# Optimization experiments

Hardware: AMD Instinct MI355X
Metric: run time of the kernel (lower is better)

Reference implementation:

```python
import jax, jax.numpy as jnp
import numpy as np

N_QUBITS = 12
N_LAYERS = 4
BATCH = 4096
DIM = 2 ** N_QUBITS  # 4096


def _apply_1q(state, U, q):
    """Apply 2x2 complex gate U to qubit q. state: (B,) + (2,)*n, wire 0 = MSB (axis q+1)."""
    state = jnp.moveaxis(state, q + 1, -1)
    state = state @ U.T
    return jnp.moveaxis(state, -1, q + 1)


def _apply_cnot(state, c, t):
    """CNOT with control c, target t: flip target amplitudes where control bit == 1."""
    flipped = jnp.flip(state, axis=t + 1)
    shape = [2 if i == c + 1 else 1 for i in range(state.ndim)]
    ctrl = jnp.arange(2).reshape(shape)
    return jnp.where(ctrl == 1, flipped, state)


def setup_inputs() -> dict:
    key = jax.random.key(0)
    k1, k2 = jax.random.split(key)
    x = jax.random.normal(k1, (BATCH, DIM), dtype=jnp.float32)
    weights = jax.random.normal(k2, (N_LAYERS, N_QUBITS, 2), dtype=jnp.float32) * 0.1
    return {"x": x, "weights": weights}


def reference(x, weights):
    n, L = N_QUBITS, N_LAYERS
    B = x.shape[0]
    # AmplitudeEmbedding with normalize=True
    norm = jnp.linalg.norm(x, axis=-1, keepdims=True)
    state = (x / norm).astype(jnp.complex64).reshape((B,) + (2,) * n)
    for layer in range(L):
        for q in range(n):
            ty = weights[layer, q, 0]
            tz = weights[layer, q, 1]
            c, s = jnp.cos(ty / 2), jnp.sin(ty / 2)
            em = jnp.exp(-0.5j * tz.astype(jnp.complex64))  # e^{-i tz/2}
            ep = jnp.exp(+0.5j * tz.astype(jnp.complex64))
            # U = RZ(tz) @ RY(ty), fused single 2x2 gate per qubit
            U = jnp.stack([
                jnp.stack([c * em, -s * em]),
                jnp.stack([s * ep, c * ep]),
            ]).astype(jnp.complex64)
            state = _apply_1q(state, U, q)
        for q in range(n - 1):
            state = _apply_cnot(state, q, q + 1)
        if n > 2:
            state = _apply_cnot(state, n - 1, 0)
    probs = jnp.abs(state) ** 2  # (B,) + (2,)*n, float32
    reduce_axes = tuple(range(1, probs.ndim))
    outs = []
    for q in range(n):
        shape = [2 if i == q + 1 else 1 for i in range(probs.ndim)]
        sign = jnp.array([1.0, -1.0], dtype=probs.dtype).reshape(shape)
        outs.append(jnp.sum(probs * sign, axis=reduce_axes))
    return jnp.stack(outs, axis=-1)  # (B, n_qubits) <Z_q> expvals
```

## Files before the change

kernel.cpp:

```cpp
#include <hip/hip_runtime.h>

#define NQ   12
#define DIM  4096
#define NL   4
#define BLK  256

typedef unsigned short u16;
typedef unsigned int   u32;
typedef float f2 __attribute__((ext_vector_type(2)));
typedef float f4v __attribute__((ext_vector_type(4)));

struct L12 { u16 b[NQ]; };

static constexpr u32 lap(const L12& A, u32 x){ u32 r=0; for(int p=0;p<NQ;++p) if((x>>p)&1u) r^=A.b[p]; return r; }
static constexpr L12 lcomp(const L12& A, const L12& B){ L12 r{}; for(int p=0;p<NQ;++p) r.b[p]=(u16)lap(A,(u32)B.b[p]); return r; }
static constexpr L12 lident(){ L12 r{}; for(int p=0;p<NQ;++p) r.b[p]=(u16)(1u<<p); return r; }

static constexpr u32 applyT(u32 i){
  i ^= ((i>>0)&1u) << 11;
  for(int q=10;q>=0;--q){ int pc=11-q, pt=10-q; i ^= ((i>>pc)&1u) << pt; }
  return i;
}
static constexpr L12 lT(){ L12 t{}; for(int p=0;p<NQ;++p) t.b[p]=(u16)applyT(1u<<p); return t; }

static constexpr L12 linv(const L12& A){
  u16 v[NQ]; u16 u[NQ];
  for(int p=0;p<NQ;++p){ v[p]=A.b[p]; u[p]=(u16)(1u<<p); }
  for(int t=0;t<NQ;++t){
    int p=t; while(!((v[p]>>t)&1u)) ++p;
    u16 tv=v[p]; v[p]=v[t]; v[t]=tv; u16 tu=u[p]; u[p]=u[t]; u[t]=tu;
    for(int k=0;k<NQ;++k) if(k!=t && ((v[k]>>t)&1u)){ v[k]^=v[t]; u[k]^=u[t]; }
  }
  L12 r{}; for(int p=0;p<NQ;++p) r.b[p]=u[p]; return r;
}
static constexpr L12 ltr(const L12& A){
  L12 r{}; for(int p=0;p<NQ;++p) for(int q=0;q<NQ;++q) if((A.b[p]>>q)&1u) r.b[q]=(u16)(r.b[q]|(1u<<p));
  return r;
}
static constexpr int cpop(u32 v){ int n=0; while(v){ n+=(int)(v&1u); v>>=1; } return n; }

struct Tables {
  u16 cm[12][16];
  u16 wg[12][4];
  u16 sp[12][4];
  u16 wexp[NQ];
};

static constexpr Tables make_tables(){
  Tables tb{};
  const L12 T   = lT();
  const L12 Tit = ltr(linv(T));
  L12 A = lident();
  L12 W = lident();
  for(int l=0;l<NL;++l){
    for(int g=0;g<3;++g){
      const int st = l*3+g;
      u16 mm[4]={0,0,0,0};
      for(int i=0;i<4;++i){ mm[i]=A.b[4*g+i]; tb.wg[st][i]=W.b[4*g+i]; }
      u32 ech[4]={0,0,0,0}; int piv[4]={0,0,0,0};
      for(int i=0;i<4;++i){
        u32 v=mm[i];
        for(int k=0;k<i;++k) if((v>>piv[k])&1u) v^=ech[k];
        int t2=11; while(!((v>>t2)&1u)) --t2;
        piv[i]=t2; ech[i]=v;
      }
      for(int a2=0;a2<4;++a2) for(int b2=a2+1;b2<4;++b2)
        if(piv[b2]<piv[a2]){ int tt=piv[a2]; piv[a2]=piv[b2]; piv[b2]=tt; }
      for(int i=0;i<4;++i) tb.sp[st][i]=(u16)piv[i];
      for(int c=0;c<16;++c){ u32 m=0; for(int i=0;i<4;++i) if((c>>i)&1) m^=mm[i]; tb.cm[st][c]=(u16)m; }
    }
    A = lcomp(A, T);
    W = lcomp(W, Tit);
  }
  for(int p=0;p<NQ;++p) tb.wexp[p]=W.b[p];
  return tb;
}

static constexpr u16 UIMG[12] = {1,2,4,8, 3,5,6,7, 9,10,11,13};

static constexpr u32 swz(u32 j){
  u32 f=0;
  for(int k=4;k<12;++k) if((j>>k)&1u) f ^= (u32)UIMG[k];
  return j ^ (f & 15u);
}

static constexpr int rankbits(const u16* v, int n, u16 mask){
  u16 bas[4]={0,0,0,0}; int r=0;
  for(int i=0;i<n;++i){
    u16 x=(u16)(v[i]&mask);
    for(int it=0; it<5 && x; ++it){
      int hb=3; while(hb>0 && !((x>>hb)&1u)) --hb;
      if(bas[hb]) x=(u16)(x^bas[hb]); else { bas[hb]=x; ++r; x=0; }
    }
  }
  return r;
}

struct Derived {
  u32 lane_c[12][8];
  u32 smb[12][4];
  u32 scmb[12][16];
  u32 g0lane[8];
  u32 u11lane[8];
  u32 u11smb[4];
  u16 pm[12];
  u16 mu[12];
};

static constexpr Derived make_derived(){
  const Tables tb = make_tables();
  Derived d{};
  for(int st=0; st<12; ++st){
    bool isp[12]={false,false,false,false,false,false,false,false,false,false,false,false};
    for(int i=0;i<4;++i) isp[tb.sp[st][i]]=true;
    int np[8]; int nn=0;
    for(int p=0;p<12;++p) if(!isp[p]) np[nn++]=p;
    u16 img8[8];
    for(int j=0;j<8;++j) img8[j]=(u16)(swz(1u<<np[j])&15u);
    int ord[8]={0,1,2,3,4,5,6,7}; bool okf=false;
    for(int a=0;a<8&&!okf;++a)for(int b=a+1;b<8&&!okf;++b)
    for(int c2=b+1;c2<8&&!okf;++c2)for(int dd=c2+1;dd<8&&!okf;++dd){
      u16 four[4]={img8[a],img8[b],img8[c2],img8[dd]};
      if(rankbits(four,4,15)!=4) continue;
      const int ids[4]={a,b,c2,dd};
      for(int ex=0; ex<4 && !okf; ++ex){
        u16 tri[3]; int tj=0;
        for(int j=0;j<4;++j) if(j!=ex) tri[tj++]=four[j];
        if(rankbits(tri,3,7)!=3) continue;
        int pp=0;
        for(int j=0;j<4;++j) if(j!=ex) ord[pp++]=ids[j];
        ord[3]=ids[ex];
        int rp=4;
        for(int j=0;j<8;++j){
          bool used=false; for(int k2=0;k2<4;++k2) if(ids[k2]==j) used=true;
          if(!used) ord[rp++]=j;
        }
        okf=true;
      }
    }
    for(int k=0;k<8;++k){
      const int pos = np[ord[k]];
      const u32 addr = swz(1u<<pos)<<4;
      u32 nib=0;
      for(int i=0;i<4;++i) nib |= (u32)((tb.wg[st][i]>>pos)&1u)<<i;
      d.lane_c[st][k] = addr | (nib<<28);
      if(st==0)  d.g0lane[k]  = 1u<<pos;
      if(st==11) d.u11lane[k] = 1u<<pos;
    }
    for(int i=0;i<4;++i)  d.smb[st][i]  = swz((u32)tb.cm[st][1<<i])<<4;
    for(int c=0;c<16;++c) d.scmb[st][c] = swz((u32)tb.cm[st][c])<<4;
    if(st==11) for(int i=0;i<4;++i) d.u11smb[i] = (u32)tb.cm[11][1<<i];
  }
  for(int q=0;q<12;++q){
    d.pm[q] = tb.wexp[11-q];
    u32 m=0;
    for(int i=0;i<4;++i) m |= (u32)(cpop((u32)tb.cm[11][1u<<i] & (u32)tb.wexp[11-q])&1)<<i;
    d.mu[q]=(u16)m;
  }
  return d;
}

__device__ constexpr Derived DV = make_derived();

__device__ __forceinline__ f2 pkfma(f2 a, f2 b, f2 c){
  f2 d;
  asm("v_pk_fma_f32 %0, %1, %2, %3" : "=v"(d) : "v"(a), "v"(b), "v"(c));
  return d;
}

template<int ST, bool WITHW>
__device__ __forceinline__ void gates(f2 (&R)[16], f2 (&I)[16], const float4* __restrict__ gw){
#pragma unroll
  for(int i=0;i<4;++i){
    const float4 g = gw[ST*4+i];
    const f2 mt  = {g.x, g.x};
    const f2 sy  = {g.y, g.y};
    const f2 mgz = {g.z, g.z};
    const f2 sw  = {g.w, g.w};
#pragma unroll
    for(int c=0;c<16;++c){
      if((c>>i)&1) continue;
      const int c1 = c|(1<<i);
      f2 uR = pkfma(mt, R[c1], R[c]);
      f2 uI = pkfma(mt, I[c1], I[c]);
      f2 vR = pkfma(sy, uR, R[c1]);
      f2 vI = pkfma(sy, uI, I[c1]);
      R[c] = pkfma(mt, vR, uR);
      I[c] = pkfma(mt, vI, uI);
      if(WITHW){
        const f2 tr = pkfma(mgz, vI, vR);
        vI = pkfma(sw, tr, vI);
        vR = pkfma(mgz, vI, tr);
      }
      R[c1]=vR; I[c1]=vI;
    }
  }
}

template<int ST, bool WITHW>
__device__ __forceinline__ void mid_step(const u32* msk, char* lds, const float4* __restrict__ gw){
  u32 acc=0;
#pragma unroll
  for(int k=0;k<8;++k) acc ^= DV.lane_c[ST][k]&msk[k];
  const u32 nib = acc>>28;
  u32 base = acc & 0x0FFFFFFFu;
#pragma unroll
  for(int i=0;i<4;++i) base ^= DV.smb[ST][i] & (0u-((nib>>i)&1u));
  u32 ad[16]; f2 R[16], I[16];
#pragma unroll
  for(int c=0;c<16;++c){
    ad[c] = base ^ DV.scmb[ST][c];
    const f4v v = *(const f4v*)(lds+ad[c]);
    R[c]=v.lo; I[c]=v.hi;
  }
  gates<ST,WITHW>(R,I,gw);
#pragma unroll
  for(int c=0;c<16;++c){ f4v v; v.lo=R[c]; v.hi=I[c]; *(f4v*)(lds+ad[c]) = v; }
  __syncthreads();
}

__global__ void prep_kernel(const float* __restrict__ w, float4* __restrict__ gw){
  const int t = threadIdx.x;
  if(t < NL*NQ){
    const int l=t/NQ, p=t%NQ, q=(NQ-1)-p;
    const float ty=w[(l*NQ+q)*2+0], tz=w[(l*NQ+q)*2+1];
    gw[t]=make_float4(-tanf(0.25f*ty), sinf(0.5f*ty), -tanf(0.5f*tz), sinf(tz));
  }
}

__global__ __launch_bounds__(BLK, 2) void qsim_kernel(const float* __restrict__ x,
                                                      const float4* __restrict__ gw,
                                                      float* __restrict__ out)
{
  __shared__ f4v st4[DIM];
  char* lds = (char*)st4;
  const int tid = threadIdx.x;
  const int bb  = blockIdx.x;

  u32 msk[8];
#pragma unroll
  for(int k=0;k<8;++k) msk[k]=0u-((u32)(tid>>k)&1u);

  u32 rep0=0, acc0=0;
#pragma unroll
  for(int k=0;k<8;++k){ rep0 ^= DV.g0lane[k]&msk[k]; acc0 ^= DV.lane_c[0][k]&msk[k]; }
  const u32 base0 = acc0 & 0x0FFFFFFFu;

  f2 R[16], I[16];
  const float* xr0 = x + (size_t)(2*bb)*DIM + rep0;
  const float* xr1 = xr0 + DIM;
#pragma unroll
  for(int s=0;s<4;++s){
    const float4 v0 = *reinterpret_cast<const float4*>(xr0 + 4*s);
    const float4 v1 = *reinterpret_cast<const float4*>(xr1 + 4*s);
    R[4*s+0]=(f2){v0.x,v1.x}; R[4*s+1]=(f2){v0.y,v1.y};
    R[4*s+2]=(f2){v0.z,v1.z}; R[4*s+3]=(f2){v0.w,v1.w};
    I[4*s+0]=(f2){0.f,0.f};   I[4*s+1]=(f2){0.f,0.f};
    I[4*s+2]=(f2){0.f,0.f};   I[4*s+3]=(f2){0.f,0.f};
  }
  gates<0,true>(R,I,gw);
#pragma unroll
  for(int c=0;c<16;++c){ f4v v; v.lo=R[c]; v.hi=I[c];
    *(f4v*)(lds + (base0 ^ DV.scmb[0][c])) = v; }
  __syncthreads();

  mid_step<1,true >(msk,lds,gw);
  mid_step<2,true >(msk,lds,gw);
  mid_step<3,true >(msk,lds,gw);
  mid_step<4,true >(msk,lds,gw);
  mid_step<5,true >(msk,lds,gw);
  mid_step<6,true >(msk,lds,gw);
  mid_step<7,true >(msk,lds,gw);
  mid_step<8,true >(msk,lds,gw);
  mid_step<9,false>(msk,lds,gw);
  mid_step<10,false>(msk,lds,gw);

  {
    u32 acc=0, urep=0;
#pragma unroll
    for(int k=0;k<8;++k){ acc ^= DV.lane_c[11][k]&msk[k]; urep ^= DV.u11lane[k]&msk[k]; }
    const u32 nib = acc>>28;
    u32 base = acc & 0x0FFFFFFFu;
#pragma unroll
    for(int i=0;i<4;++i){ const u32 mi=0u-((nib>>i)&1u); base ^= DV.smb[11][i]&mi; urep ^= DV.u11smb[i]&mi; }
#pragma unroll
    for(int c=0;c<16;++c){
      const f4v v = *(const f4v*)(lds + (base ^ DV.scmb[11][c]));
      R[c]=v.lo; I[c]=v.hi;
    }
    gates<11,false>(R,I,gw);

    f2 pr[16];
#pragma unroll
    for(int c=0;c<16;++c) pr[c]=pkfma(R[c],R[c], pkfma(I[c],I[c],(f2){0.f,0.f}));
    const f2 mone = {-1.f,-1.f};
#pragma unroll
    for(int b=1;b<16;b<<=1){
#pragma unroll
      for(int c=0;c<16;++c){
        if(c&b) continue;
        const f2 u=pr[c], v=pr[c|b];
        pr[c]=u+v;
        pr[c|b]=pkfma(v,mone,u);
      }
    }
    f2 accq[12];
#pragma unroll
    for(int q=0;q<12;++q){
      const u32 sb = ((u32)__popc(urep & (u32)DV.pm[q]) & 1u)<<31;
      const f2 a = pr[DV.mu[q]];
      accq[q]=(f2){__uint_as_float(__float_as_uint(a.x)^sb),
                   __uint_as_float(__float_as_uint(a.y)^sb)};
    }
    f2 nrm2 = pr[0];
#pragma unroll
    for(int o=32;o;o>>=1){
      nrm2.x += __shfl_xor(nrm2.x,o);
      nrm2.y += __shfl_xor(nrm2.y,o);
#pragma unroll
      for(int q=0;q<12;++q){
        accq[q].x += __shfl_xor(accq[q].x,o);
        accq[q].y += __shfl_xor(accq[q].y,o);
      }
    }
    __syncthreads();
    f2* wredp = (f2*)lds;
    const int wid=tid>>6;
    if((tid&63)==0){
#pragma unroll
      for(int q=0;q<12;++q) wredp[wid*13+q]=accq[q];
      wredp[wid*13+12]=nrm2;
    }
    __syncthreads();
    if(tid<NQ){
      const f2 s0=wredp[0*13+tid]+wredp[1*13+tid]+wredp[2*13+tid]+wredp[3*13+tid];
      const f2 sn=wredp[0*13+12]+wredp[1*13+12]+wredp[2*13+12]+wredp[3*13+12];
      out[(size_t)(2*bb+0)*NQ+tid]=s0.x/sn.x;
      out[(size_t)(2*bb+1)*NQ+tid]=s0.y/sn.y;
    }
  }
}

extern "C" void kernel_launch(void* const* d_in, const int* in_sizes, int n_in,
                              void* d_out, int out_size, void* d_ws, size_t ws_size,
                              hipStream_t stream) {
  const float* x = (const float*)d_in[0];
  const float* w = (const float*)d_in[1];
  float* out = (float*)d_out;
  float4* gw = (float4*)d_ws;
  const int B = in_sizes[0] / DIM;
  prep_kernel<<<1, 64, 0, stream>>>(w, gw);
  qsim_kernel<<<B/2, BLK, 0, stream>>>(x, gw, out);
}
```

Baseline: 114.9 us.

## Split each 4-qubit stage across lane pairs with DPP exchange, 512 threads

Each thread now holds 8 amplitudes instead of 16 and the block grows to 512 threads. One of the four qubits per stage is mapped to adjacent lanes, and its gate is applied with DPP quad-permute exchanges plus a lane-dependent sign. The aim is to cut register pressure and raise occupancy and parallelism. In exchange it adds per-stage cross-lane traffic, extra multiplies for the lane gate, and twice as many waves taking part in each barrier. Packed FMA inline asm is also replaced with elementwise fma builtins.

```diff
diff --git a/kernel.cpp b/kernel.cpp
--- a/kernel.cpp
+++ b/kernel.cpp
@@ -3,7 +3,7 @@
 #define NQ   12
 #define DIM  4096
 #define NL   4
-#define BLK  256
+#define BLK  512
 
 typedef unsigned short u16;
 typedef unsigned int   u32;
@@ -97,12 +97,13 @@
 }
 
 struct Derived {
-  u32 lane_c[12][8];
-  u32 smb[12][4];
-  u32 scmb[12][16];
-  u32 g0lane[8];
-  u32 u11lane[8];
-  u32 u11smb[4];
+  u32 lane_c[12][9];
+  u32 smb[12][3];
+  u32 scmb[12][8];
+  u32 g0lane[9];
+  u32 u0smb[3];
+  u32 u11lane[9];
+  u32 u11smb[3];
   u16 pm[12];
   u16 mu[12];
 };
@@ -110,51 +111,52 @@
 static constexpr Derived make_derived(){
   const Tables tb = make_tables();
   Derived d{};
+  u16 mm11[4]={0,0,0,0};
   for(int st=0; st<12; ++st){
+    u16 mm[4];
+    for(int i=0;i<4;++i) mm[i]=tb.cm[st][1u<<i];
+    if(st==11) for(int i=0;i<4;++i) mm11[i]=mm[i];
     bool isp[12]={false,false,false,false,false,false,false,false,false,false,false,false};
     for(int i=0;i<4;++i) isp[tb.sp[st][i]]=true;
     int np[8]; int nn=0;
     for(int p=0;p<12;++p) if(!isp[p]) np[nn++]=p;
-    u16 img8[8];
-    for(int j=0;j<8;++j) img8[j]=(u16)(swz(1u<<np[j])&15u);
-    int ord[8]={0,1,2,3,4,5,6,7}; bool okf=false;
-    for(int a=0;a<8&&!okf;++a)for(int b=a+1;b<8&&!okf;++b)
-    for(int c2=b+1;c2<8&&!okf;++c2)for(int dd=c2+1;dd<8&&!okf;++dd){
-      u16 four[4]={img8[a],img8[b],img8[c2],img8[dd]};
-      if(rankbits(four,4,15)!=4) continue;
-      const int ids[4]={a,b,c2,dd};
-      for(int ex=0; ex<4 && !okf; ++ex){
-        u16 tri[3]; int tj=0;
-        for(int j=0;j<4;++j) if(j!=ex) tri[tj++]=four[j];
-        if(rankbits(tri,3,7)!=3) continue;
-        int pp=0;
-        for(int j=0;j<4;++j) if(j!=ex) ord[pp++]=ids[j];
-        ord[3]=ids[ex];
-        int rp=4;
-        for(int j=0;j<8;++j){
-          bool used=false; for(int k2=0;k2<4;++k2) if(ids[k2]==j) used=true;
-          if(!used) ord[rp++]=j;
-        }
-        okf=true;
-      }
-    }
-    for(int k=0;k<8;++k){
-      const int pos = np[ord[k]];
-      const u32 addr = swz(1u<<pos)<<4;
+    u16 img[8];
+    for(int j=0;j<8;++j) img[j]=(u16)(swz(1u<<np[j])&15u);
+    const u16 img0=(u16)(swz((u32)mm[3])&15u);
+    int b1=0,b2=1,b3=2,best=-1;
+    for(int i1=0;i1<8;++i1)for(int i2=0;i2<8;++i2)for(int i3=0;i3<8;++i3){
+      if(i1==i2||i1==i3||i2==i3) continue;
+      u16 t8[3]={img0,img[i1],img[i2]};
+      u16 t16[4]={img0,img[i1],img[i2],img[i3]};
+      const int sc = rankbits(t16,4,15)*10 + rankbits(t8,3,7);
+      if(sc>best){ best=sc; b1=i1;b2=i2;b3=i3; }
+    }
+    int ord[8]={b1,b2,b3,0,0,0,0,0}; int rp=3;
+    for(int j=0;j<8;++j){ if(j!=b1&&j!=b2&&j!=b3) ord[rp++]=j; }
+    d.lane_c[st][0] = (swz((u32)mm[3])<<4) | (8u<<28);
+    if(st==0)  d.g0lane[0]=(u32)mm[3];
+    if(st==11) d.u11lane[0]=(u32)mm[3];
+    for(int k=1;k<9;++k){
+      const int pos=np[ord[k-1]];
       u32 nib=0;
-      for(int i=0;i<4;++i) nib |= (u32)((tb.wg[st][i]>>pos)&1u)<<i;
-      d.lane_c[st][k] = addr | (nib<<28);
-      if(st==0)  d.g0lane[k]  = 1u<<pos;
-      if(st==11) d.u11lane[k] = 1u<<pos;
-    }
-    for(int i=0;i<4;++i)  d.smb[st][i]  = swz((u32)tb.cm[st][1<<i])<<4;
-    for(int c=0;c<16;++c) d.scmb[st][c] = swz((u32)tb.cm[st][c])<<4;
-    if(st==11) for(int i=0;i<4;++i) d.u11smb[i] = (u32)tb.cm[11][1<<i];
+      for(int i=0;i<4;++i) nib|=(u32)((tb.wg[st][i]>>pos)&1u)<<i;
+      d.lane_c[st][k]=(swz(1u<<pos)<<4)|(nib<<28);
+      if(st==0)  d.g0lane[k]=1u<<pos;
+      if(st==11) d.u11lane[k]=1u<<pos;
+    }
+    for(int i=0;i<3;++i) d.smb[st][i]=swz((u32)mm[i])<<4;
+    for(int c=0;c<8;++c){
+      u32 m=0;
+      for(int i=0;i<3;++i) if((c>>i)&1) m^=(u32)mm[i];
+      d.scmb[st][c]=swz(m)<<4;
+    }
+    if(st==0)  for(int i=0;i<3;++i) d.u0smb[i]=(u32)mm[i];
+    if(st==11) for(int i=0;i<3;++i) d.u11smb[i]=(u32)mm[i];
   }
   for(int q=0;q<12;++q){
-    d.pm[q] = tb.wexp[11-q];
+    d.pm[q]=tb.wexp[11-q];
     u32 m=0;
-    for(int i=0;i<4;++i) m |= (u32)(cpop((u32)tb.cm[11][1u<<i] & (u32)tb.wexp[11-q])&1)<<i;
+    for(int i=0;i<3;++i) m|=(u32)(cpop((u32)mm11[i]&(u32)tb.wexp[11-q])&1)<<i;
     d.mu[q]=(u16)m;
   }
   return d;
@@ -162,35 +164,31 @@
 
 __device__ constexpr Derived DV = make_derived();
 
-__device__ __forceinline__ f2 pkfma(f2 a, f2 b, f2 c){
-  f2 d;
-  asm("v_pk_fma_f32 %0, %1, %2, %3" : "=v"(d) : "v"(a), "v"(b), "v"(c));
-  return d;
-}
+__device__ __forceinline__ float dppx(float v){
+  return __int_as_float(__builtin_amdgcn_mov_dpp(__float_as_int(v), 0xB1, 0xF, 0xF, true));
+}
+__device__ __forceinline__ f2 dpp2(f2 v){ f2 r; r.x=dppx(v.x); r.y=dppx(v.y); return r; }
 
 template<int ST, bool WITHW>
-__device__ __forceinline__ void gates(f2 (&R)[16], f2 (&I)[16], const float4* __restrict__ gw){
-#pragma unroll
-  for(int i=0;i<4;++i){
-    const float4 g = gw[ST*4+i];
-    const f2 mt  = {g.x, g.x};
-    const f2 sy  = {g.y, g.y};
-    const f2 mgz = {g.z, g.z};
-    const f2 sw  = {g.w, g.w};
-#pragma unroll
-    for(int c=0;c<16;++c){
+__device__ __forceinline__ void reg_gates(f2 (&R)[8], f2 (&I)[8], const float4* __restrict__ gwS){
+#pragma unroll
+  for(int i=0;i<3;++i){
+    const float4 g = gwS[ST*4+i];
+    const f2 mt={g.x,g.x}, sy={g.y,g.y}, mtz={-g.z,-g.z}, sz={g.w,g.w};
+#pragma unroll
+    for(int c=0;c<8;++c){
       if((c>>i)&1) continue;
-      const int c1 = c|(1<<i);
-      f2 uR = pkfma(mt, R[c1], R[c]);
-      f2 uI = pkfma(mt, I[c1], I[c]);
-      f2 vR = pkfma(sy, uR, R[c1]);
-      f2 vI = pkfma(sy, uI, I[c1]);
-      R[c] = pkfma(mt, vR, uR);
-      I[c] = pkfma(mt, vI, uI);
+      const int c1=c|(1<<i);
+      f2 uR=__builtin_elementwise_fma(mt,R[c1],R[c]);
+      f2 uI=__builtin_elementwise_fma(mt,I[c1],I[c]);
+      f2 vR=__builtin_elementwise_fma(sy,uR,R[c1]);
+      f2 vI=__builtin_elementwise_fma(sy,uI,I[c1]);
+      R[c]=__builtin_elementwise_fma(mt,vR,uR);
+      I[c]=__builtin_elementwise_fma(mt,vI,uI);
       if(WITHW){
-        const f2 tr = pkfma(mgz, vI, vR);
-        vI = pkfma(sw, tr, vI);
-        vR = pkfma(mgz, vI, tr);
+        f2 t=__builtin_elementwise_fma(mtz,vI,vR);
+        vI=__builtin_elementwise_fma(sz,t,vI);
+        vR=__builtin_elementwise_fma(mtz,vI,t);
       }
       R[c1]=vR; I[c1]=vI;
     }
@@ -198,38 +196,66 @@
 }
 
 template<int ST, bool WITHW>
-__device__ __forceinline__ void mid_step(const u32* msk, char* lds, const float4* __restrict__ gw){
+__device__ __forceinline__ void lane_gate(f2 (&R)[8], f2 (&I)[8], const float4* __restrict__ gwD, u32 r3m){
+  const float4 g = gwD[ST];
+  const float sg = __uint_as_float(__float_as_uint(g.y) ^ r3m ^ 0x80000000u);
+  const f2 vcy={g.x,g.x}, vsy={sg,sg};
+  const float en = r3m ? 1.f : 0.f;
+  const f2 vmtz={-g.z*en,-g.z*en}, vsz={g.w*en,g.w*en};
+#pragma unroll
+  for(int c=0;c<8;++c){
+    const f2 Rp=dpp2(R[c]), Ip=dpp2(I[c]);
+    f2 nR=__builtin_elementwise_fma(vcy,R[c],vsy*Rp);
+    f2 nI=__builtin_elementwise_fma(vcy,I[c],vsy*Ip);
+    if(WITHW){
+      f2 t=__builtin_elementwise_fma(vmtz,nI,nR);
+      nI=__builtin_elementwise_fma(vsz,t,nI);
+      nR=__builtin_elementwise_fma(vmtz,nI,t);
+    }
+    R[c]=nR; I[c]=nI;
+  }
+}
+
+template<int ST, bool WITHW>
+__device__ __forceinline__ void mid_step(const u32* msk, char* lds,
+                                         const float4* __restrict__ gwS,
+                                         const float4* __restrict__ gwD){
   u32 acc=0;
 #pragma unroll
-  for(int k=0;k<8;++k) acc ^= DV.lane_c[ST][k]&msk[k];
+  for(int k=0;k<9;++k) acc ^= DV.lane_c[ST][k]&msk[k];
   const u32 nib = acc>>28;
   u32 base = acc & 0x0FFFFFFFu;
 #pragma unroll
-  for(int i=0;i<4;++i) base ^= DV.smb[ST][i] & (0u-((nib>>i)&1u));
-  u32 ad[16]; f2 R[16], I[16];
-#pragma unroll
-  for(int c=0;c<16;++c){
-    ad[c] = base ^ DV.scmb[ST][c];
-    const f4v v = *(const f4v*)(lds+ad[c]);
+  for(int i=0;i<3;++i) base ^= DV.smb[ST][i] & (0u-((nib>>i)&1u));
+  const u32 r3m = (nib&8u)<<28;
+  u32 ad[8]; f2 R[8], I[8];
+#pragma unroll
+  for(int c=0;c<8;++c){
+    ad[c]=base^DV.scmb[ST][c];
+    const f4v v=*(const f4v*)(lds+ad[c]);
     R[c]=v.lo; I[c]=v.hi;
   }
-  gates<ST,WITHW>(R,I,gw);
-#pragma unroll
-  for(int c=0;c<16;++c){ f4v v; v.lo=R[c]; v.hi=I[c]; *(f4v*)(lds+ad[c]) = v; }
+  reg_gates<ST,WITHW>(R,I,gwS);
+  lane_gate<ST,WITHW>(R,I,gwD,r3m);
+#pragma unroll
+  for(int c=0;c<8;++c){ f4v v; v.lo=R[c]; v.hi=I[c]; *(f4v*)(lds+ad[c])=v; }
   __syncthreads();
 }
 
-__global__ void prep_kernel(const float* __restrict__ w, float4* __restrict__ gw){
+__global__ void prep_kernel(const float* __restrict__ w, float4* __restrict__ gwS,
+                            float4* __restrict__ gwD){
   const int t = threadIdx.x;
   if(t < NL*NQ){
     const int l=t/NQ, p=t%NQ, q=(NQ-1)-p;
     const float ty=w[(l*NQ+q)*2+0], tz=w[(l*NQ+q)*2+1];
-    gw[t]=make_float4(-tanf(0.25f*ty), sinf(0.5f*ty), -tanf(0.5f*tz), sinf(tz));
-  }
-}
-
-__global__ __launch_bounds__(BLK, 2) void qsim_kernel(const float* __restrict__ x,
-                                                      const float4* __restrict__ gw,
+    gwS[t]=make_float4(-tanf(0.25f*ty), sinf(0.5f*ty), tanf(0.5f*tz), sinf(tz));
+    if((p&3)==3) gwD[t>>2]=make_float4(cosf(0.5f*ty), sinf(0.5f*ty), tanf(0.5f*tz), sinf(tz));
+  }
+}
+
+__global__ __launch_bounds__(BLK, 4) void qsim_kernel(const float* __restrict__ x,
+                                                      const float4* __restrict__ gwS,
+                                                      const float4* __restrict__ gwD,
                                                       float* __restrict__ out)
 {
   __shared__ f4v st4[DIM];
@@ -237,71 +263,77 @@
   const int tid = threadIdx.x;
   const int bb  = blockIdx.x;
 
-  u32 msk[8];
-#pragma unroll
-  for(int k=0;k<8;++k) msk[k]=0u-((u32)(tid>>k)&1u);
+  u32 msk[9];
+#pragma unroll
+  for(int k=0;k<9;++k) msk[k]=0u-((u32)(tid>>k)&1u);
 
   u32 rep0=0, acc0=0;
 #pragma unroll
-  for(int k=0;k<8;++k){ rep0 ^= DV.g0lane[k]&msk[k]; acc0 ^= DV.lane_c[0][k]&msk[k]; }
-  const u32 base0 = acc0 & 0x0FFFFFFFu;
-
-  f2 R[16], I[16];
+  for(int k=0;k<9;++k){ rep0 ^= DV.g0lane[k]&msk[k]; acc0 ^= DV.lane_c[0][k]&msk[k]; }
+  const u32 nib0 = acc0>>28;
+  u32 base0 = acc0 & 0x0FFFFFFFu;
+#pragma unroll
+  for(int i=0;i<3;++i){ const u32 mi=0u-((nib0>>i)&1u); base0^=DV.smb[0][i]&mi; rep0^=DV.u0smb[i]&mi; }
+  const u32 r3m0 = (nib0&8u)<<28;
+
+  f2 R[8], I[8];
   const float* xr0 = x + (size_t)(2*bb)*DIM + rep0;
   const float* xr1 = xr0 + DIM;
-#pragma unroll
-  for(int s=0;s<4;++s){
-    const float4 v0 = *reinterpret_cast<const float4*>(xr0 + 4*s);
-    const float4 v1 = *reinterpret_cast<const float4*>(xr1 + 4*s);
-    R[4*s+0]=(f2){v0.x,v1.x}; R[4*s+1]=(f2){v0.y,v1.y};
-    R[4*s+2]=(f2){v0.z,v1.z}; R[4*s+3]=(f2){v0.w,v1.w};
-    I[4*s+0]=(f2){0.f,0.f};   I[4*s+1]=(f2){0.f,0.f};
-    I[4*s+2]=(f2){0.f,0.f};   I[4*s+3]=(f2){0.f,0.f};
-  }
-  gates<0,true>(R,I,gw);
-#pragma unroll
-  for(int c=0;c<16;++c){ f4v v; v.lo=R[c]; v.hi=I[c];
+  {
+    const float4 a0=*reinterpret_cast<const float4*>(xr0);
+    const float4 a1=*reinterpret_cast<const float4*>(xr0+4);
+    const float4 b0=*reinterpret_cast<const float4*>(xr1);
+    const float4 b1=*reinterpret_cast<const float4*>(xr1+4);
+    R[0]=(f2){a0.x,b0.x}; R[1]=(f2){a0.y,b0.y}; R[2]=(f2){a0.z,b0.z}; R[3]=(f2){a0.w,b0.w};
+    R[4]=(f2){a1.x,b1.x}; R[5]=(f2){a1.y,b1.y}; R[6]=(f2){a1.z,b1.z}; R[7]=(f2){a1.w,b1.w};
+#pragma unroll
+    for(int c=0;c<8;++c) I[c]=(f2){0.f,0.f};
+  }
+  reg_gates<0,true>(R,I,gwS);
+  lane_gate<0,true>(R,I,gwD,r3m0);
+#pragma unroll
+  for(int c=0;c<8;++c){ f4v v; v.lo=R[c]; v.hi=I[c];
     *(f4v*)(lds + (base0 ^ DV.scmb[0][c])) = v; }
   __syncthreads();
 
-  mid_step<1,true >(msk,lds,gw);
-  mid_step<2,true >(msk,lds,gw);
-  mid_step<3,true >(msk,lds,gw);
-  mid_step<4,true >(msk,lds,gw);
-  mid_step<5,true >(msk,lds,gw);
-  mid_step<6,true >(msk,lds,gw);
-  mid_step<7,true >(msk,lds,gw);
-  mid_step<8,true >(msk,lds,gw);
-  mid_step<9,false>(msk,lds,gw);
-  mid_step<10,false>(msk,lds,gw);
+  mid_step<1,true >(msk,lds,gwS,gwD);
+  mid_step<2,true >(msk,lds,gwS,gwD);
+  mid_step<3,true >(msk,lds,gwS,gwD);
+  mid_step<4,true >(msk,lds,gwS,gwD);
+  mid_step<5,true >(msk,lds,gwS,gwD);
+  mid_step<6,true >(msk,lds,gwS,gwD);
+  mid_step<7,true >(msk,lds,gwS,gwD);
+  mid_step<8,true >(msk,lds,gwS,gwD);
+  mid_step<9,false>(msk,lds,gwS,gwD);
+  mid_step<10,false>(msk,lds,gwS,gwD);
 
   {
     u32 acc=0, urep=0;
 #pragma unroll
-    for(int k=0;k<8;++k){ acc ^= DV.lane_c[11][k]&msk[k]; urep ^= DV.u11lane[k]&msk[k]; }
+    for(int k=0;k<9;++k){ acc ^= DV.lane_c[11][k]&msk[k]; urep ^= DV.u11lane[k]&msk[k]; }
     const u32 nib = acc>>28;
     u32 base = acc & 0x0FFFFFFFu;
 #pragma unroll
-    for(int i=0;i<4;++i){ const u32 mi=0u-((nib>>i)&1u); base ^= DV.smb[11][i]&mi; urep ^= DV.u11smb[i]&mi; }
-#pragma unroll
-    for(int c=0;c<16;++c){
+    for(int i=0;i<3;++i){ const u32 mi=0u-((nib>>i)&1u); base ^= DV.smb[11][i]&mi; urep ^= DV.u11smb[i]&mi; }
+    const u32 r3m = (nib&8u)<<28;
+#pragma unroll
+    for(int c=0;c<8;++c){
       const f4v v = *(const f4v*)(lds + (base ^ DV.scmb[11][c]));
       R[c]=v.lo; I[c]=v.hi;
     }
-    gates<11,false>(R,I,gw);
-
-    f2 pr[16];
-#pragma unroll
-    for(int c=0;c<16;++c) pr[c]=pkfma(R[c],R[c], pkfma(I[c],I[c],(f2){0.f,0.f}));
-    const f2 mone = {-1.f,-1.f};
-#pragma unroll
-    for(int b=1;b<16;b<<=1){
-#pragma unroll
-      for(int c=0;c<16;++c){
+    reg_gates<11,false>(R,I,gwS);
+    lane_gate<11,false>(R,I,gwD,r3m);
+
+    f2 pr[8];
+#pragma unroll
+    for(int c=0;c<8;++c) pr[c]=__builtin_elementwise_fma(R[c],R[c], I[c]*I[c]);
+#pragma unroll
+    for(int b=1;b<8;b<<=1){
+#pragma unroll
+      for(int c=0;c<8;++c){
         if(c&b) continue;
         const f2 u=pr[c], v=pr[c|b];
-        pr[c]=u+v;
-        pr[c|b]=pkfma(v,mone,u);
+        pr[c]=u+v; pr[c|b]=u-v;
       }
     }
     f2 accq[12];
@@ -333,8 +365,9 @@
     }
     __syncthreads();
     if(tid<NQ){
-      const f2 s0=wredp[0*13+tid]+wredp[1*13+tid]+wredp[2*13+tid]+wredp[3*13+tid];
-      const f2 sn=wredp[0*13+12]+wredp[1*13+12]+wredp[2*13+12]+wredp[3*13+12];
+      f2 s0=(f2){0.f,0.f}, sn=(f2){0.f,0.f};
+#pragma unroll
+      for(int wv=0;wv<8;++wv){ s0+=wredp[wv*13+tid]; sn+=wredp[wv*13+12]; }
       out[(size_t)(2*bb+0)*NQ+tid]=s0.x/sn.x;
       out[(size_t)(2*bb+1)*NQ+tid]=s0.y/sn.y;
     }
@@ -347,8 +380,9 @@
   const float* x = (const float*)d_in[0];
   const float* w = (const float*)d_in[1];
   float* out = (float*)d_out;
-  float4* gw = (float4*)d_ws;
+  float4* gwS = (float4*)d_ws;
+  float4* gwD = gwS + NL*NQ;
   const int B = in_sizes[0] / DIM;
-  prep_kernel<<<1, 64, 0, stream>>>(w, gw);
-  qsim_kernel<<<B/2, BLK, 0, stream>>>(x, gw, out);
-}
+  prep_kernel<<<1, 64, 0, stream>>>(w, gwS, gwD);
+  qsim_kernel<<<B/2, BLK, 0, stream>>>(x, gwS, gwD, out);
+}
```

After: 124.7 us. 8.6% more time.
